# Optimization experiments

Measured on AMD Instinct MI355X. Metric: run time of the kernel, lower is better.

The kernel has to match this reference:

```python
import jax, jax.numpy as jnp
import numpy as np

B, H, N1 = 2, 32, 1024  # N1 = N + 1 (extra global token row/col sliced off)
N = N1 - 1


def setup_inputs() -> dict:
    key = jax.random.key(0)
    ks = jax.random.split(key, 6)
    x = jax.random.normal(ks[0], (B, N, 3), dtype=jnp.float32)
    qk = jax.random.normal(ks[1], (B, H, N1, N1), dtype=jnp.float32)
    W1 = jax.random.normal(ks[2], (H, H), dtype=jnp.float32) * 0.1
    b1 = jax.random.normal(ks[3], (H,), dtype=jnp.float32) * 0.1
    W2 = jax.random.normal(ks[4], (1, H), dtype=jnp.float32) * 0.1
    b2 = jax.random.normal(ks[5], (1,), dtype=jnp.float32) * 0.1
    return {"x": x, "qk": qk, "W1": W1, "b1": b1, "W2": W2, "b2": b2}


def reference(x, qk, W1, b1, W2, b2):
    # qk: [B,H,N+1,N+1] -> [B,N,N,H]
    q = jnp.transpose(qk, (0, 2, 3, 1))[:, 1:, 1:, :]
    q = jnp.where(jnp.isinf(q), jnp.zeros_like(q), q)
    h = jnp.einsum('bijh,gh->bijg', q, W1) + b1            # qk_linear
    c = jnp.einsum('bijh,oh->bijo', jax.nn.relu(h), W2) + b2  # [B,N,N,1] scalar gate
    rel_pos = x[:, :, None, :] - x[:, None, :, :]          # [B,N,N,3]
    x_new = jnp.sum(rel_pos * c, axis=-2)                  # reduce over neighbor j
    return x + x_new
```

## Files before the change

kernel.cpp:

```cpp
#include <hip/hip_runtime.h>
#include <hip/hip_bf16.h>

#define Bc 2
#define Hc 32
#define N1c 1024
#define Nc 1023
#define BLOCK 256
#define PLANE (N1c * N1c)
#define LDSW 40

typedef __attribute__((ext_vector_type(8))) short bf16x8;
typedef __attribute__((ext_vector_type(4))) float f32x4;

__device__ __forceinline__ unsigned short f2bf(float a) {
    unsigned ua = __float_as_uint(a);
    ua = (ua + 0x7fffu + ((ua >> 16) & 1u)) >> 16;
    return (unsigned short)ua;
}

__global__ __launch_bounds__(BLOCK, 3) void se3_head_kernel(
    const float* __restrict__ x,
    const float* __restrict__ qk,
    const float* __restrict__ W1,
    const float* __restrict__ b1,
    const float* __restrict__ W2,
    const float* __restrict__ b2,
    float* __restrict__ out)
{
    __shared__ unsigned short qs[2][256][LDSW];
    __shared__ float xs[N1c][3];
    __shared__ float red[4][4];

    const int bi   = blockIdx.x;
    const int b    = bi / Nc;
    const int i    = bi % Nc;
    const int t    = threadIdx.x;
    const int w    = t >> 6;
    const int lane = t & 63;
    const int jl   = lane & 15;
    const int lk   = lane >> 4;

    const float* qk_row = qk + (size_t)b * Hc * PLANE + (size_t)(i + 1) * N1c;
    const float* xb     = x + (size_t)b * Nc * 3;

    for (int rr = t; rr < N1c; rr += BLOCK) {
        float v0 = 0.f, v1 = 0.f, v2 = 0.f;
        if (rr >= 1) { v0 = xb[(rr-1)*3]; v1 = xb[(rr-1)*3+1]; v2 = xb[(rr-1)*3+2]; }
        xs[rr][0] = v0; xs[rr][1] = v1; xs[rr][2] = v2;
    }

    bf16x8 B0, B1;
    #pragma unroll
    for (int e = 0; e < 8; ++e) {
        ((unsigned short*)&B0)[e] = f2bf(W1[jl * Hc + lk*8 + e]);
        ((unsigned short*)&B1)[e] = f2bf(W1[(jl + 16) * Hc + lk*8 + e]);
    }
    const float w2a = W2[jl], w2b = W2[jl + 16];
    const float bb0 = b1[jl], bb1 = b1[jl + 16];
    const f32x4 cb0 = {bb0, bb0, bb0, bb0};
    const f32x4 cb1 = {bb1, bb1, bb1, bb1};
    const float b2s = b2[0] * (1.0f / 16.0f);

    float S = 0.f, T0 = 0.f, T1 = 0.f, T2 = 0.f;
    float rA[Hc], rB[Hc];

    auto L = [&](float (&r)[Hc], int k) {
        const float* p = qk_row + k * 256 + t;
        #pragma unroll
        for (int h = 0; h < Hc; ++h)
            r[h] = p[(size_t)h * PLANE];
    };

    auto STAGE = [&](const float (&r)[Hc], int buf) {
        #pragma unroll
        for (int q4 = 0; q4 < 4; ++q4) {
            unsigned pk[4];
            #pragma unroll
            for (int e = 0; e < 4; ++e) {
                __hip_bfloat162 h2 = __float22bfloat162_rn(
                    make_float2(r[q4*8 + 2*e], r[q4*8 + 2*e + 1]));
                pk[e] = *reinterpret_cast<unsigned*>(&h2);
            }
            *reinterpret_cast<uint4*>(&qs[buf][t][q4*8]) =
                make_uint4(pk[0], pk[1], pk[2], pk[3]);
        }
    };

    auto COMP = [&](int k, int buf) {
        #pragma unroll
        for (int m = 0; m < 4; ++m) {
            const int row = w * 64 + m * 16;
            bf16x8 A = *reinterpret_cast<const bf16x8*>(&qs[buf][row + jl][lk*8]);
            f32x4 c0 = __builtin_amdgcn_mfma_f32_16x16x32_bf16(A, B0, cb0, 0, 0, 0);
            f32x4 c1 = __builtin_amdgcn_mfma_f32_16x16x32_bf16(A, B1, cb1, 0, 0, 0);
            const int jb = k * 256 + row + lk * 4;
            const float* xp = &xs[jb][0];
            f32x4 xA = *reinterpret_cast<const f32x4*>(xp);
            f32x4 xB = *reinterpret_cast<const f32x4*>(xp + 4);
            f32x4 xC = *reinterpret_cast<const f32x4*>(xp + 8);
            const float xj[4][3] = {{xA.x, xA.y, xA.z}, {xA.w, xB.x, xB.y},
                                    {xB.z, xB.w, xC.x}, {xC.y, xC.z, xC.w}};
            #pragma unroll
            for (int r = 0; r < 4; ++r) {
                float cp = fmaf(fmaxf(c0[r], 0.f), w2a,
                             fmaf(fmaxf(c1[r], 0.f), w2b, b2s));
                if (k == 0 && m == 0)
                    cp = (jb + r == 0) ? 0.f : cp;
                S += cp;
                T0 = fmaf(xj[r][0], cp, T0);
                T1 = fmaf(xj[r][1], cp, T1);
                T2 = fmaf(xj[r][2], cp, T2);
            }
        }
    };

    L(rA, 0); L(rB, 1);
    STAGE(rA, 0);
    __syncthreads();

    L(rA, 2);
    COMP(0, 0);
    STAGE(rB, 1);
    __syncthreads();

    L(rB, 3);
    COMP(1, 1);
    STAGE(rA, 0);
    __syncthreads();

    COMP(2, 0);
    STAGE(rB, 1);
    __syncthreads();

    COMP(3, 1);

    #pragma unroll
    for (int off = 32; off > 0; off >>= 1) {
        S  += __shfl_down(S,  off);
        T0 += __shfl_down(T0, off);
        T1 += __shfl_down(T1, off);
        T2 += __shfl_down(T2, off);
    }
    if (lane == 0) { red[w][0] = S; red[w][1] = T0; red[w][2] = T1; red[w][3] = T2; }
    __syncthreads();

    if (t == 0) {
        float s = 0.f, u0 = 0.f, u1 = 0.f, u2 = 0.f;
        #pragma unroll
        for (int q = 0; q < 4; ++q) {
            s += red[q][0]; u0 += red[q][1]; u1 += red[q][2]; u2 += red[q][3];
        }
        const float xi0 = xs[i+1][0], xi1 = xs[i+1][1], xi2 = xs[i+1][2];
        out[(b*Nc + i)*3 + 0] = fmaf(xi0, s, xi0) - u0;
        out[(b*Nc + i)*3 + 1] = fmaf(xi1, s, xi1) - u1;
        out[(b*Nc + i)*3 + 2] = fmaf(xi2, s, xi2) - u2;
    }
}

extern "C" void kernel_launch(void* const* d_in, const int* in_sizes, int n_in,
                              void* d_out, int out_size, void* d_ws, size_t ws_size,
                              hipStream_t stream) {
    const float* x  = (const float*)d_in[0];
    const float* qk = (const float*)d_in[1];
    const float* W1 = (const float*)d_in[2];
    const float* b1 = (const float*)d_in[3];
    const float* W2 = (const float*)d_in[4];
    const float* b2 = (const float*)d_in[5];
    float* out = (float*)d_out;

    se3_head_kernel<<<dim3(Bc * Nc), dim3(BLOCK), 0, stream>>>(
        x, qk, W1, b1, W2, b2, out);
}
```

Measured before the change: 54.11 us.

## Split head loads across thread halves with smaller j-tiles to raise occupancy

Each thread now loads 16 heads instead of 32 for a 128-wide j tile, with the two thread halves covering the two head halves. The work becomes 8 double-buffered steps instead of 4, which halves the staging registers and the LDS tile so the launch bound can rise from 3 to 4 waves per SIMD. The aim is more memory-level parallelism on the bandwidth-bound qk read. The cost is twice as many barriers and shorter bursts per load.

Result: faster. 48.47 us, median of 2 (-10.4%).

```diff
diff --git a/kernel.cpp b/kernel.cpp
--- a/kernel.cpp
+++ b/kernel.cpp
@@ -7,6 +7,8 @@
 #define Nc 1023
 #define BLOCK 256
 #define PLANE (N1c * N1c)
+#define JT 128
+#define NT 8
 #define LDSW 40
 
 typedef __attribute__((ext_vector_type(8))) short bf16x8;
@@ -18,7 +20,7 @@
     return (unsigned short)ua;
 }
 
-__global__ __launch_bounds__(BLOCK, 3) void se3_head_kernel(
+__global__ __launch_bounds__(BLOCK, 4) void se3_head_kernel(
     const float* __restrict__ x,
     const float* __restrict__ qk,
     const float* __restrict__ W1,
@@ -27,7 +29,7 @@
     const float* __restrict__ b2,
     float* __restrict__ out)
 {
-    __shared__ unsigned short qs[2][256][LDSW];
+    __shared__ unsigned short qs[2][JT][LDSW];
     __shared__ float xs[N1c][3];
     __shared__ float red[4][4];
 
@@ -39,6 +41,8 @@
     const int lane = t & 63;
     const int jl   = lane & 15;
     const int lk   = lane >> 4;
+    const int jt   = t & 127;
+    const int hh   = t >> 7;
 
     const float* qk_row = qk + (size_t)b * Hc * PLANE + (size_t)(i + 1) * N1c;
     const float* xb     = x + (size_t)b * Nc * 3;
@@ -62,18 +66,20 @@
     const float b2s = b2[0] * (1.0f / 16.0f);
 
     float S = 0.f, T0 = 0.f, T1 = 0.f, T2 = 0.f;
-    float rA[Hc], rB[Hc];
+    float rA[16], rB[16];
 
-    auto L = [&](float (&r)[Hc], int k) {
-        const float* p = qk_row + k * 256 + t;
+    const float* qbase = qk_row + jt + (size_t)(hh * 16) * PLANE;
+    auto L = [&](float (&r)[16], int k) {
+        const float* p = qbase + k * JT;
         #pragma unroll
-        for (int h = 0; h < Hc; ++h)
+        for (int h = 0; h < 16; ++h)
             r[h] = p[(size_t)h * PLANE];
     };
 
-    auto STAGE = [&](const float (&r)[Hc], int buf) {
+    auto STAGE = [&](const float (&r)[16], int buf) {
+        unsigned short* dst = &qs[buf][jt][hh * 16];
         #pragma unroll
-        for (int q4 = 0; q4 < 4; ++q4) {
+        for (int q4 = 0; q4 < 2; ++q4) {
             unsigned pk[4];
             #pragma unroll
             for (int e = 0; e < 4; ++e) {
@@ -81,19 +87,19 @@
                     make_float2(r[q4*8 + 2*e], r[q4*8 + 2*e + 1]));
                 pk[e] = *reinterpret_cast<unsigned*>(&h2);
             }
-            *reinterpret_cast<uint4*>(&qs[buf][t][q4*8]) =
+            *reinterpret_cast<uint4*>(dst + q4*8) =
                 make_uint4(pk[0], pk[1], pk[2], pk[3]);
         }
     };
 
     auto COMP = [&](int k, int buf) {
         #pragma unroll
-        for (int m = 0; m < 4; ++m) {
-            const int row = w * 64 + m * 16;
+        for (int m = 0; m < 2; ++m) {
+            const int row = w * 32 + m * 16;
             bf16x8 A = *reinterpret_cast<const bf16x8*>(&qs[buf][row + jl][lk*8]);
             f32x4 c0 = __builtin_amdgcn_mfma_f32_16x16x32_bf16(A, B0, cb0, 0, 0, 0);
             f32x4 c1 = __builtin_amdgcn_mfma_f32_16x16x32_bf16(A, B1, cb1, 0, 0, 0);
-            const int jb = k * 256 + row + lk * 4;
+            const int jb = k * JT + row + lk * 4;
             const float* xp = &xs[jb][0];
             f32x4 xA = *reinterpret_cast<const f32x4*>(xp);
             f32x4 xB = *reinterpret_cast<const f32x4*>(xp + 4);
@@ -118,21 +124,18 @@
     STAGE(rA, 0);
     __syncthreads();
 
-    L(rA, 2);
-    COMP(0, 0);
-    STAGE(rB, 1);
-    __syncthreads();
-
-    L(rB, 3);
-    COMP(1, 1);
-    STAGE(rA, 0);
-    __syncthreads();
-
-    COMP(2, 0);
-    STAGE(rB, 1);
-    __syncthreads();
-
-    COMP(3, 1);
+    #pragma unroll
+    for (int k = 0; k < NT; ++k) {
+        const int buf = k & 1;
+        if (k + 2 < NT) {
+            if (buf == 0) L(rA, k + 2); else L(rB, k + 2);
+        }
+        COMP(k, buf);
+        if (k + 1 < NT) {
+            if (buf == 0) STAGE(rB, 1); else STAGE(rA, 0);
+            __syncthreads();
+        }
+    }
 
     #pragma unroll
     for (int off = 32; off > 0; off >>= 1) {
```
